# Performance work log

Measured on AMD Instinct MI355X. Metric: run time of the kernel, lower is better.

The kernel has to match this reference:

```python
import jax, jax.numpy as jnp
import numpy as np

B, T, F, H = 4096, 512, 25, 64


def setup_inputs() -> dict:
    key = jax.random.key(0)
    ks = jax.random.split(key, 7)
    s = 0.1
    return {
        "x": jax.random.normal(ks[0], (B, T, F), dtype=jnp.float32),
        "mask": jnp.ones((B, T), dtype=jnp.float32),
        "Wx_w": jax.random.normal(ks[1], (4 * H, F), dtype=jnp.float32) * s,
        "Wx_b": jax.random.normal(ks[2], (4 * H,), dtype=jnp.float32) * s,
        "Wh_w": jax.random.normal(ks[3], (4 * H, H), dtype=jnp.float32) * s,
        "Wh_b": jax.random.normal(ks[4], (4 * H,), dtype=jnp.float32) * s,
        "fc_w": jax.random.normal(ks[5], (1, H), dtype=jnp.float32) * s,
        "fc_b": jax.random.normal(ks[6], (1,), dtype=jnp.float32) * s,
    }


def reference(x, mask, Wx_w, Wx_b, Wh_w, Wh_b, fc_w, fc_b):
    # x: [B,T,F]. Precompute input projection for all timesteps in one GEMM.
    xz = jnp.einsum("btf,gf->btg", x, Wx_w) + Wx_b  # [B,T,4H]
    xz_t = jnp.swapaxes(xz, 0, 1)  # [T,B,4H]

    def step(carry, z_x):
        h, c = carry
        z = z_x + h @ Wh_w.T + Wh_b  # [B,4H]
        i, f, g, o = jnp.split(z, 4, axis=-1)
        i = jax.nn.sigmoid(i)
        f = jax.nn.sigmoid(f)
        o = jax.nn.sigmoid(o)
        g = jnp.tanh(g)
        c_t = f * c + i * g
        h_t = o * jnp.tanh(c_t)
        return (h_t, c_t), h_t

    h0 = jnp.zeros((x.shape[0], Wh_w.shape[1]), dtype=x.dtype)
    c0 = jnp.zeros_like(h0)
    (h_last, _), _ = jax.lax.scan(step, (h0, c0), xz_t)
    # use_masked_last=False -> last timestep hidden; dropout is identity (eval)
    logits = (h_last @ fc_w.T + fc_b).squeeze(-1)  # [B]
    return logits
```

## Files before the change

### kernel.cpp

```cpp
#include <hip/hip_runtime.h>
#include <math.h>

namespace {

constexpr int TSTEPS = 512;
constexpr int F_IN   = 25;
constexpr int H_DIM  = 64;
constexpr int TILE_B = 16;
constexpr int NTHR   = 256;

typedef __attribute__((ext_vector_type(8))) short bf16x8;
typedef __attribute__((ext_vector_type(4))) float f32x4;

constexpr float LOG2E  = 1.4426950408889634f;
constexpr float LOG2E2 = 2.8853900817779268f;

__device__ __forceinline__ short f2bf(float f) {
    unsigned u = __float_as_uint(f);
    unsigned r = (u + 0x7FFFu + ((u >> 16) & 1u)) >> 16;
    return (short)r;
}
__device__ __forceinline__ unsigned cvt_pk_bf16(float lo, float hi) {
    unsigned r;
    asm("v_cvt_pk_bf16_f32 %0, %1, %2" : "=v"(r) : "v"(lo), "v"(hi));
    return r;
}
__device__ __forceinline__ float exp2_neg(float x) {
    float r;
    asm("v_exp_f32 %0, -%1" : "=v"(r) : "v"(x));
    return r;
}
__device__ __forceinline__ float exp2_negabs(float x) {
    float r;
    asm("v_exp_f32 %0, -abs(%1)" : "=v"(r) : "v"(x));
    return r;
}

__device__ __forceinline__ float lstm_cell(float zi, float zf, float zg, float zo, float& c) {
    const float ei = exp2_neg(zi);
    const float ef = exp2_neg(zf);
    const float eg = exp2_negabs(zg);
    const float eo = exp2_neg(zo);
    const float r1 = __builtin_amdgcn_rcpf((1.0f + ei) * (1.0f + eg));
    const float ig = copysignf((1.0f - eg) * r1, zg);
    const float f  = __builtin_amdgcn_rcpf(1.0f + ef);
    const float cn = fmaf(c, f, ig);
    c = cn;
    const float ec = exp2_negabs(cn * LOG2E2);
    const float r3 = __builtin_amdgcn_rcpf((1.0f + eo) * (1.0f + ec));
    return copysignf((1.0f - ec) * r3, cn);
}

__global__ __launch_bounds__(NTHR)
void lstm_mfma(const float* __restrict__ x,
               const float* __restrict__ Wx_w,
               const float* __restrict__ Wx_b,
               const float* __restrict__ Wh_w,
               const float* __restrict__ Wh_b,
               const float* __restrict__ fc_w,
               const float* __restrict__ fc_b,
               float* __restrict__ out)
{
    __shared__ short a_buf[2][3][64][8];
    __shared__ float red[4][16];

    const int tid  = threadIdx.x;
    const int l    = tid & 63;
    const int wv   = tid >> 6;
    const int lrow = l & 15;
    const int lhi  = l >> 4;
    const int row0 = blockIdx.x * TILE_B;

    bf16x8 w_hi[4][3];
    #pragma unroll
    for (int g = 0; g < 4; ++g) {
        const int col = g * 64 + wv * 16 + lrow;
        const float scale = (g == 2) ? LOG2E2 : LOG2E;
        #pragma unroll
        for (int s = 0; s < 3; ++s) {
            bf16x8 hi;
            #pragma unroll
            for (int j = 0; j < 8; ++j) {
                const int k = s * 32 + lhi * 8 + j;
                float val;
                if (k < F_IN)           val = Wx_w[col * F_IN + k];
                else if (k < 89)        val = Wh_w[col * H_DIM + (k - F_IN)];
                else if (k == 89)       val = Wx_b[col] + Wh_b[col];
                else                    val = 0.0f;
                hi[j] = f2bf(val * scale);
            }
            w_hi[g][s] = hi;
        }
    }

    for (int idx = tid; idx < 2 * 3 * 64 * 8; idx += NTHR) {
        const int j    = idx & 7;
        const int lane = (idx >> 3) & 63;
        const int s    = (idx >> 9) % 3;
        const int k    = s * 32 + (lane >> 4) * 8 + j;
        ((short*)a_buf)[idx] = (k == 89) ? (short)0x3F80 : (short)0;
    }
    __syncthreads();

    const int xrow0 = tid / F_IN,          xf0 = tid % F_IN;
    const int xrow1 = (tid + 256) / F_IN,  xf1 = (tid + 256) % F_IN;
    const float* xq0 = x + (size_t)(row0 + xrow0) * TSTEPS * F_IN + xf0;
    const float* xq1 = x + (size_t)(row0 + (tid < 144 ? xrow1 : 0)) * TSTEPS * F_IN + xf1;
    const int xoff0 = ((xrow0 | ((xf0 >> 3) << 4)) * 8) + (xf0 & 7);
    const int xoff1 = ((xrow1 | ((xf1 >> 3) << 4)) * 8) + (xf1 & 7);
    short* const abase = &a_buf[0][0][0][0];

    abase[xoff0] = f2bf(xq0[0]);
    if (tid < 144) abase[xoff1] = f2bf(xq1[0]);
    __syncthreads();

    xq0 += F_IN;
    xq1 += F_IN;

    const int unit  = wv * 16 + lrow;
    const int kh    = F_IN + unit;
    const int sh    = kh >> 5;
    const int hbank = ((kh >> 3) & 3) << 4;
    const int jh    = kh & 7;

    const float fcw = fc_w[unit];
    float c[4] = {0.f, 0.f, 0.f, 0.f};
    float hq[4] = {0.f, 0.f, 0.f, 0.f};

    const f32x4 czero = {0.f, 0.f, 0.f, 0.f};

    for (int t = 0; t < TSTEPS; ++t) {
        const int p  = t & 1;
        const int pn = p ^ 1;

        bf16x8 a0 = *(const bf16x8*)&a_buf[p][0][l][0];
        bf16x8 a1 = *(const bf16x8*)&a_buf[p][1][l][0];
        bf16x8 a2 = *(const bf16x8*)&a_buf[p][2][l][0];

        float xv0 = 0.f, xv1 = 0.f;
        if (t + 1 < TSTEPS) {
            xv0 = xq0[0];
            if (tid < 144) xv1 = xq1[0];
            xq0 += F_IN;
            xq1 += F_IN;
        }

        f32x4 acc0, acc1, acc2, acc3;
        acc0 = __builtin_amdgcn_mfma_f32_16x16x32_bf16(a0, w_hi[0][0], czero, 0, 0, 0);
        acc1 = __builtin_amdgcn_mfma_f32_16x16x32_bf16(a0, w_hi[1][0], czero, 0, 0, 0);
        acc2 = __builtin_amdgcn_mfma_f32_16x16x32_bf16(a0, w_hi[2][0], czero, 0, 0, 0);
        acc3 = __builtin_amdgcn_mfma_f32_16x16x32_bf16(a0, w_hi[3][0], czero, 0, 0, 0);

        acc0 = __builtin_amdgcn_mfma_f32_16x16x32_bf16(a1, w_hi[0][1], acc0, 0, 0, 0);
        acc1 = __builtin_amdgcn_mfma_f32_16x16x32_bf16(a1, w_hi[1][1], acc1, 0, 0, 0);
        acc2 = __builtin_amdgcn_mfma_f32_16x16x32_bf16(a1, w_hi[2][1], acc2, 0, 0, 0);
        acc3 = __builtin_amdgcn_mfma_f32_16x16x32_bf16(a1, w_hi[3][1], acc3, 0, 0, 0);

        acc0 = __builtin_amdgcn_mfma_f32_16x16x32_bf16(a2, w_hi[0][2], acc0, 0, 0, 0);
        acc1 = __builtin_amdgcn_mfma_f32_16x16x32_bf16(a2, w_hi[1][2], acc1, 0, 0, 0);
        acc2 = __builtin_amdgcn_mfma_f32_16x16x32_bf16(a2, w_hi[2][2], acc2, 0, 0, 0);
        acc3 = __builtin_amdgcn_mfma_f32_16x16x32_bf16(a2, w_hi[3][2], acc3, 0, 0, 0);

        float h0 = lstm_cell(acc0[0], acc1[0], acc2[0], acc3[0], c[0]);
        float h1 = lstm_cell(acc0[1], acc1[1], acc2[1], acc3[1], c[1]);
        float h2 = lstm_cell(acc0[2], acc1[2], acc2[2], acc3[2], c[2]);
        float h3 = lstm_cell(acc0[3], acc1[3], acc2[3], acc3[3], c[3]);
        hq[0] = h0; hq[1] = h1; hq[2] = h2; hq[3] = h3;

        const unsigned u01 = cvt_pk_bf16(h0, h1);
        const unsigned u23 = cvt_pk_bf16(h2, h3);
        short* const hdst = &a_buf[pn][sh][0][0] + hbank * 8 + lhi * 32 + jh;
        hdst[0]  = (short)(u01 & 0xffffu);
        hdst[8]  = (short)(u01 >> 16);
        hdst[16] = (short)(u23 & 0xffffu);
        hdst[24] = (short)(u23 >> 16);

        if (t + 1 < TSTEPS) {
            short* const xdst = abase + pn * (3 * 64 * 8);
            xdst[xoff0] = (short)(cvt_pk_bf16(xv0, xv0) & 0xffffu);
            if (tid < 144) xdst[xoff1] = (short)(cvt_pk_bf16(xv1, xv1) & 0xffffu);
        }
        __syncthreads();
    }

    #pragma unroll
    for (int q = 0; q < 4; ++q) {
        float pq = hq[q] * fcw;
        pq += __shfl_xor(pq, 1);
        pq += __shfl_xor(pq, 2);
        pq += __shfl_xor(pq, 4);
        pq += __shfl_xor(pq, 8);
        if (lrow == 0) red[wv][lhi * 4 + q] = pq;
    }
    __syncthreads();
    if (tid < TILE_B) {
        out[row0 + tid] = red[0][tid] + red[1][tid] + red[2][tid] + red[3][tid] + fc_b[0];
    }
}

}

extern "C" void kernel_launch(void* const* d_in, const int* in_sizes, int n_in,
                              void* d_out, int out_size, void* d_ws, size_t ws_size,
                              hipStream_t stream) {
    const float* x    = (const float*)d_in[0];
    const float* Wx_w = (const float*)d_in[2];
    const float* Wx_b = (const float*)d_in[3];
    const float* Wh_w = (const float*)d_in[4];
    const float* Wh_b = (const float*)d_in[5];
    const float* fc_w = (const float*)d_in[6];
    const float* fc_b = (const float*)d_in[7];
    float* out = (float*)d_out;

    const int B    = out_size;
    const int grid = B / TILE_B;

    lstm_mfma<<<grid, NTHR, 0, stream>>>(x, Wx_w, Wx_b, Wh_w, Wh_b, fc_w, fc_b, out);
}
```

Before: 262.5 us.

## Split x-projection MFMA off the recurrent path and batch reciprocals per step

The input projection is no longer staged through shared memory. Each wave loads its own x fragment straight from global memory and computes the next step's x·Wx contribution with separate MFMAs, issued in the middle of the current step's gate math. These results then seed the accumulators for the recurrent h·Wh MFMAs, so the serial recurrent chain shrinks from 12 MFMAs to 8 and the shared-memory x writes go away. Reciprocals are also batched four at a time with a single rcp (the product trick), which cuts transcendental ops but adds multiplies and some risk of overflow or precision loss. Every wave now loads redundant x rows from global memory.

```diff
diff --git a/kernel.cpp b/kernel.cpp
--- a/kernel.cpp
+++ b/kernel.cpp
@@ -35,20 +35,33 @@
     asm("v_exp_f32 %0, -abs(%1)" : "=v"(r) : "v"(x));
     return r;
 }
-
-__device__ __forceinline__ float lstm_cell(float zi, float zf, float zg, float zo, float& c) {
-    const float ei = exp2_neg(zi);
-    const float ef = exp2_neg(zf);
-    const float eg = exp2_negabs(zg);
-    const float eo = exp2_neg(zo);
-    const float r1 = __builtin_amdgcn_rcpf((1.0f + ei) * (1.0f + eg));
-    const float ig = copysignf((1.0f - eg) * r1, zg);
-    const float f  = __builtin_amdgcn_rcpf(1.0f + ef);
-    const float cn = fmaf(c, f, ig);
-    c = cn;
-    const float ec = exp2_negabs(cn * LOG2E2);
-    const float r3 = __builtin_amdgcn_rcpf((1.0f + eo) * (1.0f + ec));
-    return copysignf((1.0f - ec) * r3, cn);
+__device__ __forceinline__ void inv4(float a0, float a1, float a2, float a3,
+                                     float& i0, float& i1, float& i2, float& i3) {
+    const float s01 = a0 * a1;
+    const float s23 = a2 * a3;
+    const float rp  = __builtin_amdgcn_rcpf(s01 * s23);
+    const float t01 = rp * s23;
+    const float t23 = rp * s01;
+    i0 = t01 * a1;
+    i1 = t01 * a0;
+    i2 = t23 * a3;
+    i3 = t23 * a2;
+}
+
+__device__ __forceinline__ bf16x8 load_xfrag(const float* __restrict__ xrow_t, int lhi) {
+    union { unsigned u[4]; bf16x8 v; } r;
+    if (lhi < 3) {
+        float tmp[8];
+        __builtin_memcpy(tmp, xrow_t + lhi * 8, 32);
+        r.u[0] = cvt_pk_bf16(tmp[0], tmp[1]);
+        r.u[1] = cvt_pk_bf16(tmp[2], tmp[3]);
+        r.u[2] = cvt_pk_bf16(tmp[4], tmp[5]);
+        r.u[3] = cvt_pk_bf16(tmp[6], tmp[7]);
+    } else {
+        r.u[0] = cvt_pk_bf16(xrow_t[24], 1.0f);
+        r.u[1] = 0; r.u[2] = 0; r.u[3] = 0;
+    }
+    return r.v;
 }
 
 __global__ __launch_bounds__(NTHR)
@@ -61,7 +74,7 @@
                const float* __restrict__ fc_b,
                float* __restrict__ out)
 {
-    __shared__ short a_buf[2][3][64][8];
+    __shared__ short h_buf[2][2][64][8];
     __shared__ float red[4][16];
 
     const int tid  = threadIdx.x;
@@ -71,115 +84,146 @@
     const int lhi  = l >> 4;
     const int row0 = blockIdx.x * TILE_B;
 
-    bf16x8 w_hi[4][3];
+    bf16x8 w_x[4], w_h[4][2];
     #pragma unroll
     for (int g = 0; g < 4; ++g) {
         const int col = g * 64 + wv * 16 + lrow;
         const float scale = (g == 2) ? LOG2E2 : LOG2E;
         #pragma unroll
-        for (int s = 0; s < 3; ++s) {
-            bf16x8 hi;
+        for (int j = 0; j < 8; ++j) {
+            const int k = lhi * 8 + j;
+            float val;
+            if (k < F_IN)       val = Wx_w[col * F_IN + k];
+            else if (k == F_IN) val = Wx_b[col] + Wh_b[col];
+            else                val = 0.0f;
+            w_x[g][j] = f2bf(val * scale);
+        }
+        #pragma unroll
+        for (int s = 0; s < 2; ++s) {
             #pragma unroll
             for (int j = 0; j < 8; ++j) {
-                const int k = s * 32 + lhi * 8 + j;
-                float val;
-                if (k < F_IN)           val = Wx_w[col * F_IN + k];
-                else if (k < 89)        val = Wh_w[col * H_DIM + (k - F_IN)];
-                else if (k == 89)       val = Wx_b[col] + Wh_b[col];
-                else                    val = 0.0f;
-                hi[j] = f2bf(val * scale);
+                const int u = s * 32 + lhi * 8 + j;
+                w_h[g][s][j] = f2bf(Wh_w[col * H_DIM + u] * scale);
             }
-            w_hi[g][s] = hi;
-        }
-    }
-
-    for (int idx = tid; idx < 2 * 3 * 64 * 8; idx += NTHR) {
-        const int j    = idx & 7;
-        const int lane = (idx >> 3) & 63;
-        const int s    = (idx >> 9) % 3;
-        const int k    = s * 32 + (lane >> 4) * 8 + j;
-        ((short*)a_buf)[idx] = (k == 89) ? (short)0x3F80 : (short)0;
-    }
+        }
+    }
+
+    for (int idx = tid; idx < 2 * 2 * 64 * 8; idx += NTHR)
+        ((short*)h_buf)[idx] = 0;
     __syncthreads();
 
-    const int xrow0 = tid / F_IN,          xf0 = tid % F_IN;
-    const int xrow1 = (tid + 256) / F_IN,  xf1 = (tid + 256) % F_IN;
-    const float* xq0 = x + (size_t)(row0 + xrow0) * TSTEPS * F_IN + xf0;
-    const float* xq1 = x + (size_t)(row0 + (tid < 144 ? xrow1 : 0)) * TSTEPS * F_IN + xf1;
-    const int xoff0 = ((xrow0 | ((xf0 >> 3) << 4)) * 8) + (xf0 & 7);
-    const int xoff1 = ((xrow1 | ((xf1 >> 3) << 4)) * 8) + (xf1 & 7);
-    short* const abase = &a_buf[0][0][0][0];
-
-    abase[xoff0] = f2bf(xq0[0]);
-    if (tid < 144) abase[xoff1] = f2bf(xq1[0]);
-    __syncthreads();
-
-    xq0 += F_IN;
-    xq1 += F_IN;
-
-    const int unit  = wv * 16 + lrow;
-    const int kh    = F_IN + unit;
-    const int sh    = kh >> 5;
-    const int hbank = ((kh >> 3) & 3) << 4;
-    const int jh    = kh & 7;
+    const float* xrow = x + (size_t)(row0 + lrow) * TSTEPS * F_IN;
+
+    const f32x4 czero = {0.f, 0.f, 0.f, 0.f};
+    f32x4 accx0, accx1, accx2, accx3;
+    {
+        const bf16x8 xf = load_xfrag(xrow, lhi);
+        accx0 = __builtin_amdgcn_mfma_f32_16x16x32_bf16(xf, w_x[0], czero, 0, 0, 0);
+        accx1 = __builtin_amdgcn_mfma_f32_16x16x32_bf16(xf, w_x[1], czero, 0, 0, 0);
+        accx2 = __builtin_amdgcn_mfma_f32_16x16x32_bf16(xf, w_x[2], czero, 0, 0, 0);
+        accx3 = __builtin_amdgcn_mfma_f32_16x16x32_bf16(xf, w_x[3], czero, 0, 0, 0);
+    }
+
+    const int unit = wv * 16 + lrow;
+    const int sh   = unit >> 5;
+    const int bank = ((unit & 31) >> 3) << 4;
+    const int jh   = unit & 7;
 
     const float fcw = fc_w[unit];
-    float c[4] = {0.f, 0.f, 0.f, 0.f};
+    float c[4]  = {0.f, 0.f, 0.f, 0.f};
     float hq[4] = {0.f, 0.f, 0.f, 0.f};
-
-    const f32x4 czero = {0.f, 0.f, 0.f, 0.f};
 
     for (int t = 0; t < TSTEPS; ++t) {
         const int p  = t & 1;
         const int pn = p ^ 1;
 
-        bf16x8 a0 = *(const bf16x8*)&a_buf[p][0][l][0];
-        bf16x8 a1 = *(const bf16x8*)&a_buf[p][1][l][0];
-        bf16x8 a2 = *(const bf16x8*)&a_buf[p][2][l][0];
-
-        float xv0 = 0.f, xv1 = 0.f;
+        float xl[8];
         if (t + 1 < TSTEPS) {
-            xv0 = xq0[0];
-            if (tid < 144) xv1 = xq1[0];
-            xq0 += F_IN;
-            xq1 += F_IN;
-        }
+            const float* px = xrow + (t + 1) * F_IN;
+            if (lhi < 3) __builtin_memcpy(xl, px + lhi * 8, 32);
+            else         xl[0] = px[24];
+        }
+
+        const bf16x8 h1 = *(const bf16x8*)&h_buf[p][0][l][0];
+        const bf16x8 h2 = *(const bf16x8*)&h_buf[p][1][l][0];
 
         f32x4 acc0, acc1, acc2, acc3;
-        acc0 = __builtin_amdgcn_mfma_f32_16x16x32_bf16(a0, w_hi[0][0], czero, 0, 0, 0);
-        acc1 = __builtin_amdgcn_mfma_f32_16x16x32_bf16(a0, w_hi[1][0], czero, 0, 0, 0);
-        acc2 = __builtin_amdgcn_mfma_f32_16x16x32_bf16(a0, w_hi[2][0], czero, 0, 0, 0);
-        acc3 = __builtin_amdgcn_mfma_f32_16x16x32_bf16(a0, w_hi[3][0], czero, 0, 0, 0);
-
-        acc0 = __builtin_amdgcn_mfma_f32_16x16x32_bf16(a1, w_hi[0][1], acc0, 0, 0, 0);
-        acc1 = __builtin_amdgcn_mfma_f32_16x16x32_bf16(a1, w_hi[1][1], acc1, 0, 0, 0);
-        acc2 = __builtin_amdgcn_mfma_f32_16x16x32_bf16(a1, w_hi[2][1], acc2, 0, 0, 0);
-        acc3 = __builtin_amdgcn_mfma_f32_16x16x32_bf16(a1, w_hi[3][1], acc3, 0, 0, 0);
-
-        acc0 = __builtin_amdgcn_mfma_f32_16x16x32_bf16(a2, w_hi[0][2], acc0, 0, 0, 0);
-        acc1 = __builtin_amdgcn_mfma_f32_16x16x32_bf16(a2, w_hi[1][2], acc1, 0, 0, 0);
-        acc2 = __builtin_amdgcn_mfma_f32_16x16x32_bf16(a2, w_hi[2][2], acc2, 0, 0, 0);
-        acc3 = __builtin_amdgcn_mfma_f32_16x16x32_bf16(a2, w_hi[3][2], acc3, 0, 0, 0);
-
-        float h0 = lstm_cell(acc0[0], acc1[0], acc2[0], acc3[0], c[0]);
-        float h1 = lstm_cell(acc0[1], acc1[1], acc2[1], acc3[1], c[1]);
-        float h2 = lstm_cell(acc0[2], acc1[2], acc2[2], acc3[2], c[2]);
-        float h3 = lstm_cell(acc0[3], acc1[3], acc2[3], acc3[3], c[3]);
-        hq[0] = h0; hq[1] = h1; hq[2] = h2; hq[3] = h3;
-
-        const unsigned u01 = cvt_pk_bf16(h0, h1);
-        const unsigned u23 = cvt_pk_bf16(h2, h3);
-        short* const hdst = &a_buf[pn][sh][0][0] + hbank * 8 + lhi * 32 + jh;
+        acc0 = __builtin_amdgcn_mfma_f32_16x16x32_bf16(h1, w_h[0][0], accx0, 0, 0, 0);
+        acc1 = __builtin_amdgcn_mfma_f32_16x16x32_bf16(h1, w_h[1][0], accx1, 0, 0, 0);
+        acc2 = __builtin_amdgcn_mfma_f32_16x16x32_bf16(h1, w_h[2][0], accx2, 0, 0, 0);
+        acc3 = __builtin_amdgcn_mfma_f32_16x16x32_bf16(h1, w_h[3][0], accx3, 0, 0, 0);
+        acc0 = __builtin_amdgcn_mfma_f32_16x16x32_bf16(h2, w_h[0][1], acc0, 0, 0, 0);
+        acc1 = __builtin_amdgcn_mfma_f32_16x16x32_bf16(h2, w_h[1][1], acc1, 0, 0, 0);
+        acc2 = __builtin_amdgcn_mfma_f32_16x16x32_bf16(h2, w_h[2][1], acc2, 0, 0, 0);
+        acc3 = __builtin_amdgcn_mfma_f32_16x16x32_bf16(h2, w_h[3][1], acc3, 0, 0, 0);
+
+        const float ei0 = exp2_neg(acc0[0]), ei1 = exp2_neg(acc0[1]),
+                    ei2 = exp2_neg(acc0[2]), ei3 = exp2_neg(acc0[3]);
+        const float ef0 = exp2_neg(acc1[0]), ef1 = exp2_neg(acc1[1]),
+                    ef2 = exp2_neg(acc1[2]), ef3 = exp2_neg(acc1[3]);
+        const float eg0 = exp2_negabs(acc2[0]), eg1 = exp2_negabs(acc2[1]),
+                    eg2 = exp2_negabs(acc2[2]), eg3 = exp2_negabs(acc2[3]);
+        const float eo0 = exp2_neg(acc3[0]), eo1 = exp2_neg(acc3[1]),
+                    eo2 = exp2_neg(acc3[2]), eo3 = exp2_neg(acc3[3]);
+
+        const float A0 = (1.f + ei0) * (1.f + eg0), A1 = (1.f + ei1) * (1.f + eg1),
+                    A2 = (1.f + ei2) * (1.f + eg2), A3 = (1.f + ei3) * (1.f + eg3);
+        float iA0, iA1, iA2, iA3;
+        inv4(A0, A1, A2, A3, iA0, iA1, iA2, iA3);
+        float f0, f1, f2, f3;
+        inv4(1.f + ef0, 1.f + ef1, 1.f + ef2, 1.f + ef3, f0, f1, f2, f3);
+
+        const float ig0 = copysignf((1.f - eg0) * iA0, acc2[0]);
+        const float ig1 = copysignf((1.f - eg1) * iA1, acc2[1]);
+        const float ig2 = copysignf((1.f - eg2) * iA2, acc2[2]);
+        const float ig3 = copysignf((1.f - eg3) * iA3, acc2[3]);
+
+        const float cn0 = fmaf(c[0], f0, ig0);
+        const float cn1 = fmaf(c[1], f1, ig1);
+        const float cn2 = fmaf(c[2], f2, ig2);
+        const float cn3 = fmaf(c[3], f3, ig3);
+        c[0] = cn0; c[1] = cn1; c[2] = cn2; c[3] = cn3;
+
+        if (t + 1 < TSTEPS) {
+            union { unsigned u[4]; bf16x8 v; } xr;
+            if (lhi < 3) {
+                xr.u[0] = cvt_pk_bf16(xl[0], xl[1]);
+                xr.u[1] = cvt_pk_bf16(xl[2], xl[3]);
+                xr.u[2] = cvt_pk_bf16(xl[4], xl[5]);
+                xr.u[3] = cvt_pk_bf16(xl[6], xl[7]);
+            } else {
+                xr.u[0] = cvt_pk_bf16(xl[0], 1.0f);
+                xr.u[1] = 0; xr.u[2] = 0; xr.u[3] = 0;
+            }
+            accx0 = __builtin_amdgcn_mfma_f32_16x16x32_bf16(xr.v, w_x[0], czero, 0, 0, 0);
+            accx1 = __builtin_amdgcn_mfma_f32_16x16x32_bf16(xr.v, w_x[1], czero, 0, 0, 0);
+            accx2 = __builtin_amdgcn_mfma_f32_16x16x32_bf16(xr.v, w_x[2], czero, 0, 0, 0);
+            accx3 = __builtin_amdgcn_mfma_f32_16x16x32_bf16(xr.v, w_x[3], czero, 0, 0, 0);
+        }
+
+        const float ec0 = exp2_negabs(cn0 * LOG2E2);
+        const float ec1 = exp2_negabs(cn1 * LOG2E2);
+        const float ec2 = exp2_negabs(cn2 * LOG2E2);
+        const float ec3 = exp2_negabs(cn3 * LOG2E2);
+        const float C0 = (1.f + eo0) * (1.f + ec0), C1 = (1.f + eo1) * (1.f + ec1),
+                    C2 = (1.f + eo2) * (1.f + ec2), C3 = (1.f + eo3) * (1.f + ec3);
+        float iC0, iC1, iC2, iC3;
+        inv4(C0, C1, C2, C3, iC0, iC1, iC2, iC3);
+
+        const float h0 = copysignf((1.f - ec0) * iC0, cn0);
+        const float h1v = copysignf((1.f - ec1) * iC1, cn1);
+        const float h2v = copysignf((1.f - ec2) * iC2, cn2);
+        const float h3v = copysignf((1.f - ec3) * iC3, cn3);
+        hq[0] = h0; hq[1] = h1v; hq[2] = h2v; hq[3] = h3v;
+
+        const unsigned u01 = cvt_pk_bf16(h0, h1v);
+        const unsigned u23 = cvt_pk_bf16(h2v, h3v);
+        short* const hdst = &h_buf[pn][sh][bank + lhi * 4][jh];
         hdst[0]  = (short)(u01 & 0xffffu);
         hdst[8]  = (short)(u01 >> 16);
         hdst[16] = (short)(u23 & 0xffffu);
         hdst[24] = (short)(u23 >> 16);
 
-        if (t + 1 < TSTEPS) {
-            short* const xdst = abase + pn * (3 * 64 * 8);
-            xdst[xoff0] = (short)(cvt_pk_bf16(xv0, xv0) & 0xffffu);
-            if (tid < 144) xdst[xoff1] = (short)(cvt_pk_bf16(xv1, xv1) & 0xffffu);
-        }
         __syncthreads();
     }
 
```

Result: slower. 416.9 us (+58.8%).

## Halve batch tile to 8 rows and split gate math across lane halves

Applied to the files above, without the earlier changes.

Each block now handles 8 batch rows instead of 16, which doubles the grid to raise occupancy and parallelism across CUs. The 16-row MFMA output is still computed, with rows 8-15 of the A operand holding unused data. Upper-half lanes take accumulator elements 2-3 through cross-lane shuffles, so each lane runs only two LSTM cells instead of four. Reciprocals are paired with a shared-rcp trick, and the last timestep is peeled so it skips the x prefetch. The trade-off is MFMA work wasted on padding rows and extra shuffles, in exchange for a shorter serial elementwise chain per step.

```diff
diff --git a/kernel.cpp b/kernel.cpp
--- a/kernel.cpp
+++ b/kernel.cpp
@@ -6,7 +6,7 @@
 constexpr int TSTEPS = 512;
 constexpr int F_IN   = 25;
 constexpr int H_DIM  = 64;
-constexpr int TILE_B = 16;
+constexpr int TILE_B = 8;
 constexpr int NTHR   = 256;
 
 typedef __attribute__((ext_vector_type(8))) short bf16x8;
@@ -35,20 +35,10 @@
     asm("v_exp_f32 %0, -abs(%1)" : "=v"(r) : "v"(x));
     return r;
 }
-
-__device__ __forceinline__ float lstm_cell(float zi, float zf, float zg, float zo, float& c) {
-    const float ei = exp2_neg(zi);
-    const float ef = exp2_neg(zf);
-    const float eg = exp2_negabs(zg);
-    const float eo = exp2_neg(zo);
-    const float r1 = __builtin_amdgcn_rcpf((1.0f + ei) * (1.0f + eg));
-    const float ig = copysignf((1.0f - eg) * r1, zg);
-    const float f  = __builtin_amdgcn_rcpf(1.0f + ef);
-    const float cn = fmaf(c, f, ig);
-    c = cn;
-    const float ec = exp2_negabs(cn * LOG2E2);
-    const float r3 = __builtin_amdgcn_rcpf((1.0f + eo) * (1.0f + ec));
-    return copysignf((1.0f - ec) * r3, cn);
+__device__ __forceinline__ void inv2(float a0, float a1, float& i0, float& i1) {
+    const float rp = __builtin_amdgcn_rcpf(a0 * a1);
+    i0 = rp * a1;
+    i1 = rp * a0;
 }
 
 __global__ __launch_bounds__(NTHR)
@@ -62,7 +52,7 @@
                float* __restrict__ out)
 {
     __shared__ short a_buf[2][3][64][8];
-    __shared__ float red[4][16];
+    __shared__ float red8[8][4];
 
     const int tid  = threadIdx.x;
     const int l    = tid & 63;
@@ -102,34 +92,32 @@
     }
     __syncthreads();
 
-    const int xrow0 = tid / F_IN,          xf0 = tid % F_IN;
-    const int xrow1 = (tid + 256) / F_IN,  xf1 = (tid + 256) % F_IN;
+    const bool xact  = tid < TILE_B * F_IN;
+    const int  xrow0 = xact ? tid / F_IN : 0;
+    const int  xf0   = xact ? tid % F_IN : 0;
     const float* xq0 = x + (size_t)(row0 + xrow0) * TSTEPS * F_IN + xf0;
-    const float* xq1 = x + (size_t)(row0 + (tid < 144 ? xrow1 : 0)) * TSTEPS * F_IN + xf1;
-    const int xoff0 = ((xrow0 | ((xf0 >> 3) << 4)) * 8) + (xf0 & 7);
-    const int xoff1 = ((xrow1 | ((xf1 >> 3) << 4)) * 8) + (xf1 & 7);
+    const int  xoff0 = ((xrow0 | ((xf0 >> 3) << 4)) * 8) + (xf0 & 7);
     short* const abase = &a_buf[0][0][0][0];
 
-    abase[xoff0] = f2bf(xq0[0]);
-    if (tid < 144) abase[xoff1] = f2bf(xq1[0]);
+    if (xact) abase[xoff0] = f2bf(xq0[0]);
     __syncthreads();
-
     xq0 += F_IN;
-    xq1 += F_IN;
 
     const int unit  = wv * 16 + lrow;
     const int kh    = F_IN + unit;
     const int sh    = kh >> 5;
     const int hbank = ((kh >> 3) & 3) << 4;
     const int jh    = kh & 7;
+    const int r0    = (lhi & 1) * 4 + ((lhi >> 1) << 1);
+    const bool lo   = (lhi < 2);
 
     const float fcw = fc_w[unit];
-    float c[4] = {0.f, 0.f, 0.f, 0.f};
-    float hq[4] = {0.f, 0.f, 0.f, 0.f};
+    float c0 = 0.f, c1 = 0.f;
+    float hq0 = 0.f, hq1 = 0.f;
 
     const f32x4 czero = {0.f, 0.f, 0.f, 0.f};
 
-    for (int t = 0; t < TSTEPS; ++t) {
+    auto step = [&](int t, bool DO_X) {
         const int p  = t & 1;
         const int pn = p ^ 1;
 
@@ -137,12 +125,10 @@
         bf16x8 a1 = *(const bf16x8*)&a_buf[p][1][l][0];
         bf16x8 a2 = *(const bf16x8*)&a_buf[p][2][l][0];
 
-        float xv0 = 0.f, xv1 = 0.f;
-        if (t + 1 < TSTEPS) {
+        float xv0 = 0.f;
+        if (DO_X && xact) {
             xv0 = xq0[0];
-            if (tid < 144) xv1 = xq1[0];
             xq0 += F_IN;
-            xq1 += F_IN;
         }
 
         f32x4 acc0, acc1, acc2, acc3;
@@ -161,40 +147,79 @@
         acc2 = __builtin_amdgcn_mfma_f32_16x16x32_bf16(a2, w_hi[2][2], acc2, 0, 0, 0);
         acc3 = __builtin_amdgcn_mfma_f32_16x16x32_bf16(a2, w_hi[3][2], acc3, 0, 0, 0);
 
-        float h0 = lstm_cell(acc0[0], acc1[0], acc2[0], acc3[0], c[0]);
-        float h1 = lstm_cell(acc0[1], acc1[1], acc2[1], acc3[1], c[1]);
-        float h2 = lstm_cell(acc0[2], acc1[2], acc2[2], acc3[2], c[2]);
-        float h3 = lstm_cell(acc0[3], acc1[3], acc2[3], acc3[3], c[3]);
-        hq[0] = h0; hq[1] = h1; hq[2] = h2; hq[3] = h3;
-
-        const unsigned u01 = cvt_pk_bf16(h0, h1);
-        const unsigned u23 = cvt_pk_bf16(h2, h3);
-        short* const hdst = &a_buf[pn][sh][0][0] + hbank * 8 + lhi * 32 + jh;
-        hdst[0]  = (short)(u01 & 0xffffu);
-        hdst[8]  = (short)(u01 >> 16);
-        hdst[16] = (short)(u23 & 0xffffu);
-        hdst[24] = (short)(u23 >> 16);
-
-        if (t + 1 < TSTEPS) {
+        const float ti2 = __shfl_xor(acc0[2], 32);
+        const float ti3 = __shfl_xor(acc0[3], 32);
+        const float tf2 = __shfl_xor(acc1[2], 32);
+        const float tf3 = __shfl_xor(acc1[3], 32);
+        const float tg2 = __shfl_xor(acc2[2], 32);
+        const float tg3 = __shfl_xor(acc2[3], 32);
+        const float to2 = __shfl_xor(acc3[2], 32);
+        const float to3 = __shfl_xor(acc3[3], 32);
+        const float zi0 = lo ? acc0[0] : ti2, zi1 = lo ? acc0[1] : ti3;
+        const float zf0 = lo ? acc1[0] : tf2, zf1 = lo ? acc1[1] : tf3;
+        const float zg0 = lo ? acc2[0] : tg2, zg1 = lo ? acc2[1] : tg3;
+        const float zo0 = lo ? acc3[0] : to2, zo1 = lo ? acc3[1] : to3;
+
+        const float ei0 = exp2_neg(zi0), ei1 = exp2_neg(zi1);
+        const float ef0 = exp2_neg(zf0), ef1 = exp2_neg(zf1);
+        const float eg0 = exp2_negabs(zg0), eg1 = exp2_negabs(zg1);
+        const float eo0 = exp2_neg(zo0), eo1 = exp2_neg(zo1);
+
+        const float A0 = (1.f + ei0) * (1.f + eg0);
+        const float A1 = (1.f + ei1) * (1.f + eg1);
+        float iA0, iA1;
+        inv2(A0, A1, iA0, iA1);
+        float f0, f1;
+        inv2(1.f + ef0, 1.f + ef1, f0, f1);
+
+        const float ig0 = copysignf((1.f - eg0) * iA0, zg0);
+        const float ig1 = copysignf((1.f - eg1) * iA1, zg1);
+
+        const float cn0 = fmaf(c0, f0, ig0);
+        const float cn1 = fmaf(c1, f1, ig1);
+        c0 = cn0; c1 = cn1;
+
+        const float ec0 = exp2_negabs(cn0 * LOG2E2);
+        const float ec1 = exp2_negabs(cn1 * LOG2E2);
+        const float C0 = (1.f + eo0) * (1.f + ec0);
+        const float C1 = (1.f + eo1) * (1.f + ec1);
+        float iC0, iC1;
+        inv2(C0, C1, iC0, iC1);
+
+        const float h0v = copysignf((1.f - ec0) * iC0, cn0);
+        const float h1v = copysignf((1.f - ec1) * iC1, cn1);
+        hq0 = h0v; hq1 = h1v;
+
+        const unsigned u01 = cvt_pk_bf16(h0v, h1v);
+        short* const hdst = &a_buf[pn][sh][0][0] + (hbank + r0) * 8 + jh;
+        hdst[0] = (short)(u01 & 0xffffu);
+        hdst[8] = (short)(u01 >> 16);
+
+        if (DO_X && xact) {
             short* const xdst = abase + pn * (3 * 64 * 8);
             xdst[xoff0] = (short)(cvt_pk_bf16(xv0, xv0) & 0xffffu);
-            if (tid < 144) xdst[xoff1] = (short)(cvt_pk_bf16(xv1, xv1) & 0xffffu);
         }
         __syncthreads();
-    }
-
+    };
+
+    for (int t = 0; t < TSTEPS - 1; ++t) step(t, true);
+    step(TSTEPS - 1, false);
+
+    float p0 = hq0 * fcw;
+    float p1 = hq1 * fcw;
     #pragma unroll
-    for (int q = 0; q < 4; ++q) {
-        float pq = hq[q] * fcw;
-        pq += __shfl_xor(pq, 1);
-        pq += __shfl_xor(pq, 2);
-        pq += __shfl_xor(pq, 4);
-        pq += __shfl_xor(pq, 8);
-        if (lrow == 0) red[wv][lhi * 4 + q] = pq;
+    for (int m = 1; m <= 8; m <<= 1) {
+        p0 += __shfl_xor(p0, m);
+        p1 += __shfl_xor(p1, m);
+    }
+    if (lrow == 0) {
+        red8[r0 + 0][wv] = p0;
+        red8[r0 + 1][wv] = p1;
     }
     __syncthreads();
     if (tid < TILE_B) {
-        out[row0 + tid] = red[0][tid] + red[1][tid] + red[2][tid] + red[3][tid] + fc_b[0];
+        out[row0 + tid] = red8[tid][0] + red8[tid][1] + red8[tid][2] + red8[tid][3]
+                        + fc_b[0];
     }
 }
 
```

Result: slower. 298.2 us (+13.6%).
